# Performance work log

Hardware: AMD Instinct MI355X
Metric: run time of the kernel (lower is better)

## Reference

```python
import jax, jax.numpy as jnp
import numpy as np

IN_OCT = 512
OUT_OCT = 512
BATCH = 512


def setup_inputs() -> dict:
    key = jax.random.key(0)
    kx, kw = jax.random.split(key)
    x = jax.random.normal(kx, (BATCH, IN_OCT * 8), dtype=jnp.float32)
    weight = jax.random.normal(kw, (OUT_OCT, IN_OCT, 8, 8), dtype=jnp.float32)
    bias = jnp.zeros((OUT_OCT, 8), dtype=jnp.float32)
    return {"x": x, "weight": weight, "bias": bias}


def reference(x, weight, bias):
    # x: [B, in_oct*8]; weight: [out_oct, in_oct, 8, 8]; bias: [out_oct, 8]
    B = x.shape[0]
    out_oct, in_oct = weight.shape[0], weight.shape[1]
    xo = x.reshape(B, in_oct, 8)
    # octonion_mul(x[:, j], weight[i, j]) applies the per-pair 8x8 octonion
    # left-multiplication matrix; summed over j it is one bilinear contraction.
    y = jnp.einsum("bjp,ijpk->bik", xo, weight) + bias[None, :, :]
    return y.reshape(B, out_oct * 8)
```

## Files before the change

kernel.cpp:

```cpp
#include <hip/hip_runtime.h>
#include <stdint.h>


#define M_DIM 512
#define N_DIM 4096
#define K_DIM 4096
#define KSPLIT 4
#define NIT ((K_DIM / KSPLIT) / 32)

typedef __bf16 bf16x8 __attribute__((ext_vector_type(8)));
typedef float f32x4 __attribute__((ext_vector_type(4)));

__device__ inline unsigned short f2bf(float f) {
  union { float f; unsigned int u; } v;
  v.f = f;
  unsigned int u = v.u;
  unsigned int r = (u + 0x7fffu + ((u >> 16) & 1u)) >> 16;
  return (unsigned short)r;
}

__global__ __launch_bounds__(256) void prep_kernel(
    const float* __restrict__ x, const float* __restrict__ w,
    const float* __restrict__ bias, unsigned short* __restrict__ abf,
    unsigned short* __restrict__ bt, float* __restrict__ out) {
  const int bid = blockIdx.x;
  const int t = threadIdx.x;
  if (bid < 4096) {
    __shared__ __align__(16) unsigned short lT[8][512];
    const int i = bid >> 3;
    const int jg = bid & 7;
    const float4* src =
        (const float4*)(w + (size_t)i * 32768 + jg * 4096 + t * 16);
    float4 v0 = src[0], v1 = src[1], v2 = src[2], v3 = src[3];
    const int jp = (t >> 2) * 8 + (t & 3) * 2;
    const float* lo = (const float*)&v0;
    const float* hi = (const float*)&v2;
#pragma unroll
    for (int k = 0; k < 4; ++k) {
      unsigned int pk =
          (unsigned int)f2bf(lo[k]) | ((unsigned int)f2bf(hi[k]) << 16);
      *(unsigned int*)&lT[k][jp] = pk;
    }
    lo = (const float*)&v1;
    hi = (const float*)&v3;
#pragma unroll
    for (int k = 0; k < 4; ++k) {
      unsigned int pk =
          (unsigned int)f2bf(lo[k]) | ((unsigned int)f2bf(hi[k]) << 16);
      *(unsigned int*)&lT[k + 4][jp] = pk;
    }
    __syncthreads();
    const int r = t >> 5, c = t & 31;
    const uint4* s = (const uint4*)&lT[r][c * 16];
    uint4* d = (uint4*)(bt + (size_t)(i * 8 + r) * K_DIM + jg * 512 + c * 16);
    d[0] = s[0];
    d[1] = s[1];
  } else if (bid < 5120) {
    int g = (bid - 4096) * 256 + t;
    const float4* xi = (const float4*)x;
    float4 a = xi[g * 2];
    float4 b = xi[g * 2 + 1];
    __attribute__((aligned(16))) unsigned short o[8] = {
        f2bf(a.x), f2bf(a.y), f2bf(a.z), f2bf(a.w),
        f2bf(b.x), f2bf(b.y), f2bf(b.z), f2bf(b.w)};
    *(uint4*)(abf + (size_t)g * 8) = *(const uint4*)o;
  } else {
    int g = (bid - 5120) * 256 + t;
    int el = g * 4;
    int col = el & (N_DIM - 1);
    *(float4*)(out + el) = *(const float4*)(bias + col);
  }
}

__device__ inline void gld16(const void* g, void* l) {
  __builtin_amdgcn_global_load_lds(
      (const __attribute__((address_space(1))) unsigned int*)g,
      (__attribute__((address_space(3))) unsigned int*)l, 16, 0, 0);
}

__global__ __launch_bounds__(512, 6) void gemm_kernel(
    const unsigned short* __restrict__ A, const unsigned short* __restrict__ Bt,
    float* __restrict__ out) {
  __shared__ __align__(16) char lds[2][12 * 1024];
  const int t = threadIdx.x;
  const int n0 = blockIdx.x * 64;
  const int m0 = blockIdx.y * 128;
  const int kc0 = blockIdx.z * (K_DIM / KSPLIT);
  const int w = t >> 6;
  const int lane = t & 63;
  const int wr = w >> 1;
  const int wc = w & 1;
  const int lrow = lane & 15;
  const int kb = lane >> 4;

  f32x4 acc[2][2] = {};

  const size_t aOff = (size_t)(m0 + (t >> 2)) * K_DIM + kc0 + (t & 3) * 8;
  const size_t bOff = (size_t)(n0 + (t >> 2)) * K_DIM + kc0 + (t & 3) * 8;

  auto issue = [&](int it) {
    char* buf = lds[it & 1];
    gld16(A + aOff + it * 32, buf + t * 16);
    if (t < 256) gld16(Bt + bOff + it * 32, buf + 8192 + t * 16);
  };

  issue(0);
  for (int it = 0; it < NIT; ++it) {
    __syncthreads();
    if (it + 1 < NIT) issue(it + 1);
    const unsigned short* cA = (const unsigned short*)lds[it & 1];
    const unsigned short* cB = cA + 4096;

    bf16x8 af[2], bfr[2];
#pragma unroll
    for (int mt = 0; mt < 2; ++mt)
      af[mt] = *(const bf16x8*)(cA + (wr * 32 + mt * 16 + lrow) * 32 + kb * 8);
#pragma unroll
    for (int nt = 0; nt < 2; ++nt)
      bfr[nt] = *(const bf16x8*)(cB + (wc * 32 + nt * 16 + lrow) * 32 + kb * 8);
#pragma unroll
    for (int mt = 0; mt < 2; ++mt)
#pragma unroll
      for (int nt = 0; nt < 2; ++nt)
        acc[mt][nt] = __builtin_amdgcn_mfma_f32_16x16x32_bf16(
            af[mt], bfr[nt], acc[mt][nt], 0, 0, 0);
  }

#pragma unroll
  for (int mt = 0; mt < 2; ++mt) {
    const int gmb = m0 + wr * 32 + mt * 16 + kb * 4;
#pragma unroll
    for (int nt = 0; nt < 2; ++nt) {
      const int gn = n0 + wc * 32 + nt * 16 + lrow;
#pragma unroll
      for (int r = 0; r < 4; ++r)
        atomicAdd(out + (size_t)(gmb + r) * N_DIM + gn, acc[mt][nt][r]);
    }
  }
}

extern "C" void kernel_launch(void* const* d_in, const int* in_sizes, int n_in,
                              void* d_out, int out_size, void* d_ws,
                              size_t ws_size, hipStream_t stream) {
  const float* x = (const float*)d_in[0];
  const float* w = (const float*)d_in[1];
  const float* bias = (const float*)d_in[2];
  float* out = (float*)d_out;

  unsigned short* abf = (unsigned short*)d_ws;
  unsigned short* bt = abf + (size_t)M_DIM * K_DIM;

  prep_kernel<<<7168, 256, 0, stream>>>(x, w, bias, abf, bt, out);

  dim3 grid(N_DIM / 64, M_DIM / 128, KSPLIT);
  gemm_kernel<<<grid, 512, 0, stream>>>(abf, bt, out);
}
```

Before: 154.7 us.

## Enlarge GEMM tile to 128x128 and replace split-K atomics with partial-sum reduction

Doubles the GEMM block tile along N to 128x128, giving each wave a 64x32 sub-tile with 8 MFMA accumulators, so each A/B fragment is reused more and fewer blocks run. When the workspace is large enough, split-K partials go to separate buffers with plain stores, and a new reduce kernel sums them and adds the bias. This replaces the bias pre-fill and the float atomics. The cost is an extra launch plus 32 MB of partial writes and reads, and lower occupancy from larger LDS and register use.

```diff
diff --git a/kernel.cpp b/kernel.cpp
--- a/kernel.cpp
+++ b/kernel.cpp
@@ -7,6 +7,7 @@
 #define K_DIM 4096
 #define KSPLIT 4
 #define NIT ((K_DIM / KSPLIT) / 32)
+#define PART_ELEMS (M_DIM * N_DIM)
 
 typedef __bf16 bf16x8 __attribute__((ext_vector_type(8)));
 typedef float f32x4 __attribute__((ext_vector_type(4)));
@@ -78,22 +79,23 @@
       (__attribute__((address_space(3))) unsigned int*)l, 16, 0, 0);
 }
 
-__global__ __launch_bounds__(512, 6) void gemm_kernel(
+__global__ __launch_bounds__(512, 4) void gemm_kernel(
     const unsigned short* __restrict__ A, const unsigned short* __restrict__ Bt,
-    float* __restrict__ out) {
-  __shared__ __align__(16) char lds[2][12 * 1024];
+    float* __restrict__ out, float* __restrict__ part, int use_atomic) {
+  __shared__ __align__(16) char lds[2][16 * 1024];
   const int t = threadIdx.x;
-  const int n0 = blockIdx.x * 64;
+  const int n0 = blockIdx.x * 128;
   const int m0 = blockIdx.y * 128;
-  const int kc0 = blockIdx.z * (K_DIM / KSPLIT);
+  const int z = blockIdx.z;
+  const int kc0 = z * (K_DIM / KSPLIT);
   const int w = t >> 6;
   const int lane = t & 63;
-  const int wr = w >> 1;
-  const int wc = w & 1;
+  const int wr = w >> 2;
+  const int wc = w & 3;
   const int lrow = lane & 15;
   const int kb = lane >> 4;
 
-  f32x4 acc[2][2] = {};
+  f32x4 acc[4][2] = {};
 
   const size_t aOff = (size_t)(m0 + (t >> 2)) * K_DIM + kc0 + (t & 3) * 8;
   const size_t bOff = (size_t)(n0 + (t >> 2)) * K_DIM + kc0 + (t & 3) * 8;
@@ -101,7 +103,7 @@
   auto issue = [&](int it) {
     char* buf = lds[it & 1];
     gld16(A + aOff + it * 32, buf + t * 16);
-    if (t < 256) gld16(Bt + bOff + it * 32, buf + 8192 + t * 16);
+    gld16(Bt + bOff + it * 32, buf + 8192 + t * 16);
   };
 
   issue(0);
@@ -111,15 +113,15 @@
     const unsigned short* cA = (const unsigned short*)lds[it & 1];
     const unsigned short* cB = cA + 4096;
 
-    bf16x8 af[2], bfr[2];
+    bf16x8 af[4], bfr[2];
 #pragma unroll
-    for (int mt = 0; mt < 2; ++mt)
-      af[mt] = *(const bf16x8*)(cA + (wr * 32 + mt * 16 + lrow) * 32 + kb * 8);
+    for (int mt = 0; mt < 4; ++mt)
+      af[mt] = *(const bf16x8*)(cA + (wr * 64 + mt * 16 + lrow) * 32 + kb * 8);
 #pragma unroll
     for (int nt = 0; nt < 2; ++nt)
       bfr[nt] = *(const bf16x8*)(cB + (wc * 32 + nt * 16 + lrow) * 32 + kb * 8);
 #pragma unroll
-    for (int mt = 0; mt < 2; ++mt)
+    for (int mt = 0; mt < 4; ++mt)
 #pragma unroll
       for (int nt = 0; nt < 2; ++nt)
         acc[mt][nt] = __builtin_amdgcn_mfma_f32_16x16x32_bf16(
@@ -127,16 +129,43 @@
   }
 
 #pragma unroll
-  for (int mt = 0; mt < 2; ++mt) {
-    const int gmb = m0 + wr * 32 + mt * 16 + kb * 4;
+  for (int mt = 0; mt < 4; ++mt) {
+    const int gmb = m0 + wr * 64 + mt * 16 + kb * 4;
 #pragma unroll
     for (int nt = 0; nt < 2; ++nt) {
       const int gn = n0 + wc * 32 + nt * 16 + lrow;
+      if (use_atomic) {
 #pragma unroll
-      for (int r = 0; r < 4; ++r)
-        atomicAdd(out + (size_t)(gmb + r) * N_DIM + gn, acc[mt][nt][r]);
+        for (int r = 0; r < 4; ++r)
+          atomicAdd(out + (size_t)(gmb + r) * N_DIM + gn, acc[mt][nt][r]);
+      } else {
+        float* p = part + (size_t)z * PART_ELEMS;
+#pragma unroll
+        for (int r = 0; r < 4; ++r)
+          p[(size_t)(gmb + r) * N_DIM + gn] = acc[mt][nt][r];
+      }
     }
   }
+}
+
+__global__ __launch_bounds__(256) void reduce_kernel(
+    const float* __restrict__ part, const float* __restrict__ bias,
+    float* __restrict__ out) {
+  const int g = blockIdx.x * 256 + threadIdx.x;
+  const float4* p = (const float4*)part;
+  const float4* b4 = (const float4*)bias;
+  const int Q = PART_ELEMS / 4;
+  float4 s0 = p[g];
+  float4 s1 = p[g + Q];
+  float4 s2 = p[g + 2 * Q];
+  float4 s3 = p[g + 3 * Q];
+  float4 bb = b4[g & (N_DIM / 4 - 1)];
+  float4 r;
+  r.x = s0.x + s1.x + s2.x + s3.x + bb.x;
+  r.y = s0.y + s1.y + s2.y + s3.y + bb.y;
+  r.z = s0.z + s1.z + s2.z + s3.z + bb.z;
+  r.w = s0.w + s1.w + s2.w + s3.w + bb.w;
+  ((float4*)out)[g] = r;
 }
 
 extern "C" void kernel_launch(void* const* d_in, const int* in_sizes, int n_in,
@@ -149,9 +178,17 @@
 
   unsigned short* abf = (unsigned short*)d_ws;
   unsigned short* bt = abf + (size_t)M_DIM * K_DIM;
+  float* part = (float*)((char*)d_ws + 36u * 1024 * 1024);
 
-  prep_kernel<<<7168, 256, 0, stream>>>(x, w, bias, abf, bt, out);
+  const bool have_ws = ws_size >= 68ull * 1024 * 1024;
+  const int use_atomic = have_ws ? 0 : 1;
 
-  dim3 grid(N_DIM / 64, M_DIM / 128, KSPLIT);
-  gemm_kernel<<<grid, 512, 0, stream>>>(abf, bt, out);
+  prep_kernel<<<use_atomic ? 7168 : 5120, 256, 0, stream>>>(x, w, bias, abf,
+                                                            bt, out);
+
+  dim3 grid(N_DIM / 128, M_DIM / 128, KSPLIT);
+  gemm_kernel<<<grid, 512, 0, stream>>>(abf, bt, out, part, use_atomic);
+
+  if (!use_atomic)
+    reduce_kernel<<<PART_ELEMS / 4 / 256, 256, 0, stream>>>(part, bias, out);
 }
```

After: 139.0 us. -10.2%, faster.
